# Optimization experiments

Hardware: AMD Instinct MI355X
Metric: run time of the kernel (lower is better)

The kernel has to match this reference:

```python
import jax, jax.numpy as jnp
import numpy as np

B, S, D, H, NS = 4, 4096, 1024, 16, 128
DA, DF = 512, 4096
DK, DV = DA // H, D // H  # 32, 64
TEMP = 1.0
EPS = 1e-6


def setup_inputs() -> dict:
    key = jax.random.key(0)
    ks = jax.random.split(key, 8)
    r = lambda k, shp: jax.random.normal(k, shp, jnp.float32) * 0.02
    return dict(
        x=jax.random.normal(ks[0], (B, S, D), jnp.float32),
        mask=jnp.ones((B, S), jnp.float32),
        residual_scale=jnp.ones((1,), jnp.float32),
        w_q=r(ks[1], (D, DA)), b_q=jnp.zeros((DA,), jnp.float32),
        w_kv=r(ks[2], (D, DA + D)), b_kv=jnp.zeros((DA + D,), jnp.float32),
        w_s=r(ks[3], (D, H * NS)), b_s=jnp.zeros((H * NS,), jnp.float32),
        w_cat=r(ks[4], (D, D)), b_cat=jnp.zeros((D,), jnp.float32),
        norm1_w=jnp.ones((D,), jnp.float32), norm2_w=jnp.ones((D,), jnp.float32),
        w1=r(ks[5], (D, DF)), b1=jnp.zeros((DF,), jnp.float32),
        w2=r(ks[6], (DF, D)), b2=jnp.zeros((D,), jnp.float32),
    )


def _rms(x, w):
    return x * jax.lax.rsqrt(jnp.mean(x * x, axis=-1, keepdims=True) + EPS) * w


def _forward(x, mask, residual_scale, w_q, b_q, w_kv, b_kv, w_s, b_s,
             w_cat, b_cat, norm1_w, norm2_w, w1, b1, w2, b2):
    neg = jnp.finfo(jnp.float32).min
    xn = _rms(x, norm1_w)
    q = (xn @ w_q + b_q).reshape(B, S, H, DK).transpose(0, 2, 1, 3)        # [B,H,S,DK]
    kv = (xn @ w_kv + b_kv).reshape(B, S, H, DK + DV).transpose(0, 2, 1, 3)  # [B,H,S,DK+DV]
    k_raw, v_raw = kv[..., :DK], kv[..., DK:]

    # DSZRC sampler: per-head soft routing of S tokens -> NS sampled KV rows
    logits = (x @ w_s + b_s).reshape(B, S, H, NS).transpose(0, 2, 3, 1)    # [B,H,NS,S]
    logits = jnp.where(mask[:, None, None, :] > 0, logits, neg)
    probs = jax.nn.softmax(logits / TEMP, axis=-1)
    kv_s = jnp.einsum('bhms,bhsd->bhmd', probs, kv)                        # [B,H,NS,DK+DV]
    k_s, v_s = kv_s[..., :DK], kv_s[..., DK:]

    # branch 1: dense SDPA over sampled KV
    scale = 1.0 / np.sqrt(DK).astype(np.float32)
    att = jax.nn.softmax(jnp.einsum('bhqd,bhkd->bhqk', q, k_s) * scale, axis=-1)
    out1 = jnp.einsum('bhqk,bhkd->bhqd', att, v_s)                         # [B,H,S,DV]

    # branch 2: fp16 sliding-window flash attn, left window = NS (keys i-NS..i)
    f16 = lambda t: t.astype(jnp.float16).astype(jnp.float32)
    qh, kh, vh = f16(q), f16(k_raw), f16(v_raw)
    bs = NS
    nb = S // bs
    qb = qh.reshape(B, H, nb, bs, DK)
    kb = kh.reshape(B, H, nb, bs, DK)
    vb = vh.reshape(B, H, nb, bs, DV)
    shift = lambda t: jnp.concatenate([jnp.zeros_like(t[:, :, :1]), t[:, :, :-1]], axis=2)
    kctx = jnp.concatenate([shift(kb), kb], axis=3)                        # [B,H,nb,2bs,DK]
    vctx = jnp.concatenate([shift(vb), vb], axis=3)
    sc = jnp.einsum('bhnad,bhnkd->bhnak', qb, kctx) * scale                # [B,H,nb,bs,2bs]
    a = jnp.arange(bs)[:, None]
    bcol = jnp.arange(2 * bs)[None, :]
    band = (bcol >= a) & (bcol <= a + NS)                                  # 0 <= q-k <= NS
    tpos = jnp.arange(nb)[:, None, None]
    valid = band[None] & ((tpos > 0) | (bcol >= bs)[None])                 # no keys before pos 0
    p = jax.nn.softmax(jnp.where(valid[None, None], sc, neg), axis=-1)
    out2 = f16(jnp.einsum('bhnak,bhnkd->bhnad', p, vctx)).reshape(B, H, S, DV)

    x_att = (out1 + out2).transpose(0, 2, 1, 3).reshape(B, S, D)
    x = x + (x_att @ w_cat + b_cat) * residual_scale
    h = _rms(x, norm2_w)
    x = x + (jax.nn.gelu(h @ w1 + b1, approximate=False) @ w2 + b2) * residual_scale
    return x


def reference(x, mask, residual_scale, w_q, b_q, w_kv, b_kv, w_s, b_s,
              w_cat, b_cat, norm1_w, norm2_w, w1, b1, w2, b2):
    return _forward(x, mask, residual_scale, w_q, b_q, w_kv, b_kv, w_s, b_s,
                    w_cat, b_cat, norm1_w, norm2_w, w1, b1, w2, b2)
```

## Files before the change

kernel.cpp:

```cpp
#include <hip/hip_runtime.h>
#include <cstdint>
#include <cmath>

#define DEV __device__ __forceinline__

using f16 = _Float16;
typedef f16  f16x4 __attribute__((ext_vector_type(4)));
typedef f16  f16x8 __attribute__((ext_vector_type(8)));
typedef float f32x4 __attribute__((ext_vector_type(4)));

constexpr int Bq = 4, Sq = 4096, Hq = 16;
constexpr int Tq = Bq * Sq;

DEV void gload_lds16(const void* g, void* l) {
  __builtin_amdgcn_global_load_lds(
      (const __attribute__((address_space(1))) void*)g,
      (__attribute__((address_space(3))) void*)l, 16, 0, 0);
}

DEV void stage_swz(const char* gbase, long gstride, char* lds, int nbytes,
                   int rowlog, int swzmask) {
  int tid = threadIdx.x;
  for (int b0 = 0; b0 < nbytes; b0 += 4096) {
    int P = b0 + tid * 16;
    int L = P ^ (((P >> rowlog) & swzmask) << 4);
    long row  = L >> rowlog;
    int  colb = L & ((1 << rowlog) - 1);
    gload_lds16(gbase + row * gstride + colb, lds + b0 + (tid & ~63) * 16);
  }
}

DEV void stage_swz512(const char* gbase, long gstride, char* lds, int nbytes,
                      int rowlog, int swzmask) {
  int tid = threadIdx.x;
  for (int b0 = 0; b0 < nbytes; b0 += 8192) {
    int P = b0 + tid * 16;
    int L = P ^ (((P >> rowlog) & swzmask) << 4);
    long row  = L >> rowlog;
    int  colb = L & ((1 << rowlog) - 1);
    gload_lds16(gbase + row * gstride + colb, lds + b0 + (tid & ~63) * 16);
  }
}

DEV float wave16_max(float v) {
#pragma unroll
  for (int d = 1; d < 16; d <<= 1) v = fmaxf(v, __shfl_xor(v, d, 64));
  return v;
}
DEV float wave16_sum(float v) {
#pragma unroll
  for (int d = 1; d < 16; d <<= 1) v += __shfl_xor(v, d, 64);
  return v;
}

__global__ __launch_bounds__(256) void wcast_k(const float* __restrict__ W,
                                               f16* __restrict__ Wt, int K, int N) {
  int n0 = blockIdx.x * 32, k0 = blockIdx.y * 32;
  __shared__ float tile[32][33];
  int tid = threadIdx.x, r = tid >> 5, c = tid & 31;
#pragma unroll
  for (int i = 0; i < 4; ++i)
    tile[r + i * 8][c] = W[(size_t)(k0 + r + i * 8) * N + n0 + c];
  __syncthreads();
#pragma unroll
  for (int i = 0; i < 4; ++i) {
    int rr = r + i * 8;
    Wt[(size_t)(n0 + rr) * K + k0 + c] = (f16)tile[c][rr];
  }
}

__global__ void bias_concat_k(const float* __restrict__ bq, const float* __restrict__ bkv,
                              float* __restrict__ out) {
  int i = blockIdx.x * 256 + threadIdx.x;
  out[i] = (i < 512) ? bq[i] : bkv[i - 512];
}

__global__ __launch_bounds__(256) void rmsnorm_k(const float* __restrict__ x,
                                                 const float* __restrict__ w,
                                                 f16* __restrict__ xn) {
  int row = blockIdx.x, tid = threadIdx.x;
  float4 v = ((const float4*)(x + (size_t)row * 1024))[tid];
  float ss = v.x * v.x + v.y * v.y + v.z * v.z + v.w * v.w;
#pragma unroll
  for (int d = 1; d < 64; d <<= 1) ss += __shfl_xor(ss, d, 64);
  __shared__ float red[4];
  if ((tid & 63) == 0) red[tid >> 6] = ss;
  __syncthreads();
  float tot = red[0] + red[1] + red[2] + red[3];
  float r = rsqrtf(tot * (1.0f / 1024.0f) + 1e-6f);
  float4 wv = ((const float4*)w)[tid];
  f16x4 o;
  o[0] = (f16)(v.x * r * wv.x); o[1] = (f16)(v.y * r * wv.y);
  o[2] = (f16)(v.z * r * wv.z); o[3] = (f16)(v.w * r * wv.w);
  *(f16x4*)(xn + (size_t)row * 1024 + tid * 4) = o;
}

template <int MODE>
__global__ __launch_bounds__(256) void gemm_k(const f16* __restrict__ A, const f16* __restrict__ Bt,
                                              const float* __restrict__ bias,
                                              float* __restrict__ outF,
                                              const float* __restrict__ resid,
                                              const float* __restrict__ rsp,
                                              int M, int N, int K, int lda, int ldb) {
  __shared__ alignas(16) char smA[2][16384];
  __shared__ alignas(16) char smB[2][16384];
  int nwgx = gridDim.x, nbc = gridDim.y;
  int bidl = blockIdx.y * nwgx + blockIdx.x;
  int cpx = (nwgx * nbc) >> 3;
  int xcd = bidl & 7, pos = bidl >> 3;
  int rpm = cpx / nbc;
  int nbi = pos / rpm, mbi = pos % rpm;
  int mb = xcd * rpm + mbi;
  long n0 = (long)nbi * 128;
  int tid = threadIdx.x, lane = tid & 63, wv = tid >> 6, wr = wv >> 1, wc = wv & 1;
  long m0 = (long)mb * 128;
  f32x4 acc[4][4] = {};

  const char* gA[4]; const char* gB[4]; int lo[4];
  long stepA = (MODE == 7) ? 524288 : 128;
  {
    const char* Abase;
    if (MODE == 7) Abase = (const char*)(A + (((m0 >> 12) * 16) * 4096 + (m0 & 4095)) * 64);
    else           Abase = (const char*)(A + m0 * lda);
    const char* Bbase = (const char*)(Bt + n0 * ldb);
    long astr = (MODE == 7) ? 128 : (long)lda * 2;
#pragma unroll
    for (int c = 0; c < 4; ++c) {
      int P = c * 4096 + tid * 16;
      int L = P ^ (((P >> 7) & 7) << 4);
      long row = L >> 7; int colb = L & 127;
      lo[c] = c * 4096 + (tid & ~63) * 16;
      gA[c] = Abase + row * astr + colb;
      gB[c] = Bbase + row * ((long)ldb * 2) + colb;
    }
  }
  auto stageAB = [&](int buf, int t) {
#pragma unroll
    for (int c = 0; c < 4; ++c) gload_lds16(gB[c] + (long)t * 128, smB[buf] + lo[c]);
#pragma unroll
    for (int c = 0; c < 4; ++c) gload_lds16(gA[c] + (long)t * stepA, smA[buf] + lo[c]);
  };

  int T = K >> 6;
  stageAB(0, 0);
  __syncthreads();
  int cur = 0;
  for (int t = 0; t < T; ++t) {
    if (t + 1 < T) stageAB(cur ^ 1, t + 1);
#pragma unroll
    for (int kk = 0; kk < 2; ++kk) {
      int kbyte = kk * 64 + (lane >> 4) * 16;
      f16x8 aF[4], bF[4];
#pragma unroll
      for (int m = 0; m < 4; ++m) {
        int L = (wr * 64 + m * 16 + (lane & 15)) * 128 + kbyte;
        aF[m] = *(const f16x8*)(smA[cur] + (L ^ (((L >> 7) & 7) << 4)));
      }
#pragma unroll
      for (int n = 0; n < 4; ++n) {
        int L = (wc * 64 + n * 16 + (lane & 15)) * 128 + kbyte;
        bF[n] = *(const f16x8*)(smB[cur] + (L ^ (((L >> 7) & 7) << 4)));
      }
#pragma unroll
      for (int m = 0; m < 4; ++m)
#pragma unroll
        for (int n = 0; n < 4; ++n)
          acc[m][n] = __builtin_amdgcn_mfma_f32_16x16x32_f16(aF[m], bF[n], acc[m][n], 0, 0, 0);
    }
    __syncthreads();
    cur ^= 1;
  }
  float rsv = rsp[0];
#pragma unroll
  for (int m = 0; m < 4; ++m)
#pragma unroll
    for (int n = 0; n < 4; ++n) {
      long gn = n0 + wc * 64 + n * 16 + (lane & 15);
      float bv = bias[gn];
      long rbase = m0 + wr * 64 + m * 16 + (lane >> 4) * 4;
#pragma unroll
      for (int i = 0; i < 4; ++i) {
        long gm = rbase + i;
        float v = acc[m][n][i] + bv;
        long idx = gm * N + gn;
        outF[idx] = resid[idx] + v * rsv;
      }
    }
}

template <int MODE>
__global__ __launch_bounds__(512) void gemm256_k(const f16* __restrict__ A, const f16* __restrict__ Bt,
                                                 const float* __restrict__ bias,
                                                 f16* __restrict__ o1, f16* __restrict__ o2,
                                                 f16* __restrict__ o3,
                                                 const float* __restrict__ resid,
                                                 int M, int N, int K, int lda, int ldb, int pp) {
  __shared__ alignas(16) char smA[2][32768];
  __shared__ alignas(16) char smB[2][32768];
  int nwgx = gridDim.x, nbc = gridDim.y;
  int bidl = blockIdx.y * nwgx + blockIdx.x;
  int cpx = (nwgx * nbc) >> 3;
  int xcd = bidl & 7, pos = bidl >> 3;
  int rpm = cpx / nbc;
  int nbi = pos / rpm, mbi = pos % rpm;
  int mb = xcd * rpm + mbi;
  long n0 = (long)nbi * 256;
  int tid = threadIdx.x, lane = tid & 63, wv = tid >> 6;
  int wr = wv >> 2, wc = wv & 3;
  long m0;
  long t0 = 0;
  int bq = 0;
  if (MODE == 5) {
    bq = mb >> 3; int sb = mb & 7;
    m0 = (long)sb * 256;
    t0 = (long)bq * 4096 + (long)pp * 2048 + m0;
  } else {
    m0 = (long)mb * 256;
  }
  f32x4 acc[8][4] = {};
  const char* Bb = (const char*)(Bt + n0 * ldb);

  if constexpr (MODE == 5) {
    auto stageAB5 = [&](int buf, int k0) {
      stage_swz512(Bb + (long)k0 * 2, (long)ldb * 2, smB[buf], 32768, 7, 7);
      int P = tid * 16;
#pragma unroll
      for (int b0 = 0; b0 < 32768; b0 += 8192) {
        int PP = b0 + P;
        int L = PP ^ (((PP >> 7) & 7) << 4);
        int row = L >> 7, colf = (L & 127) >> 1;
        const float* src = resid + (size_t)(t0 + row) * 1024 + k0 + colf;
        float4 u0 = *(const float4*)src;
        float4 u1 = *(const float4*)(src + 4);
        f16x8 o;
        o[0] = (f16)u0.x; o[1] = (f16)u0.y; o[2] = (f16)u0.z; o[3] = (f16)u0.w;
        o[4] = (f16)u1.x; o[5] = (f16)u1.y; o[6] = (f16)u1.z; o[7] = (f16)u1.w;
        *(f16x8*)(smA[buf] + PP) = o;
      }
    };
    stageAB5(0, 0);
    __syncthreads();
    int cur = 0;
    for (int k0 = 0; k0 < K; k0 += 64) {
      if (k0 + 64 < K) stageAB5(cur ^ 1, k0 + 64);
#pragma unroll
      for (int kk = 0; kk < 2; ++kk) {
        int kb2 = kk * 64 + (lane >> 4) * 16;
        f16x8 aF[8], bF[4];
#pragma unroll
        for (int m = 0; m < 8; ++m) {
          int L = (wr * 128 + m * 16 + (lane & 15)) * 128 + kb2;
          aF[m] = *(const f16x8*)(smA[cur] + (L ^ (((L >> 7) & 7) << 4)));
        }
#pragma unroll
        for (int n = 0; n < 4; ++n) {
          int L = (wc * 64 + n * 16 + (lane & 15)) * 128 + kb2;
          bF[n] = *(const f16x8*)(smB[cur] + (L ^ (((L >> 7) & 7) << 4)));
        }
#pragma unroll
        for (int m = 0; m < 8; ++m)
#pragma unroll
          for (int n = 0; n < 4; ++n)
            acc[m][n] = __builtin_amdgcn_mfma_f32_16x16x32_f16(aF[m], bF[n], acc[m][n], 0, 0, 0);
      }
      __syncthreads();
      cur ^= 1;
    }
  } else {
    const char* gA[4]; const char* gB[4]; int lo[4];
    {
      const char* Abase = (const char*)(A + m0 * lda);
#pragma unroll
      for (int c = 0; c < 4; ++c) {
        int P = c * 8192 + tid * 16;
        int L = P ^ (((P >> 7) & 7) << 4);
        long row = L >> 7; int colb = L & 127;
        lo[c] = c * 8192 + (tid & ~63) * 16;
        gA[c] = Abase + row * ((long)lda * 2) + colb;
        gB[c] = Bb + row * ((long)ldb * 2) + colb;
      }
    }
    auto stageAB = [&](int buf, int t) {
#pragma unroll
      for (int c = 0; c < 4; ++c) gload_lds16(gB[c] + (long)t * 128, smB[buf] + lo[c]);
#pragma unroll
      for (int c = 0; c < 4; ++c) gload_lds16(gA[c] + (long)t * 128, smA[buf] + lo[c]);
    };
    int T = K >> 6;
    stageAB(0, 0);
    __syncthreads();
    int cur = 0;
    for (int t = 0; t < T; ++t) {
      if (t + 1 < T) stageAB(cur ^ 1, t + 1);
#pragma unroll
      for (int kk = 0; kk < 2; ++kk) {
        int kb2 = kk * 64 + (lane >> 4) * 16;
        f16x8 aF[8], bF[4];
#pragma unroll
        for (int m = 0; m < 8; ++m) {
          int L = (wr * 128 + m * 16 + (lane & 15)) * 128 + kb2;
          aF[m] = *(const f16x8*)(smA[cur] + (L ^ (((L >> 7) & 7) << 4)));
        }
#pragma unroll
        for (int n = 0; n < 4; ++n) {
          int L = (wc * 64 + n * 16 + (lane & 15)) * 128 + kb2;
          bF[n] = *(const f16x8*)(smB[cur] + (L ^ (((L >> 7) & 7) << 4)));
        }
#pragma unroll
        for (int m = 0; m < 8; ++m)
#pragma unroll
          for (int n = 0; n < 4; ++n)
            acc[m][n] = __builtin_amdgcn_mfma_f32_16x16x32_f16(aF[m], bF[n], acc[m][n], 0, 0, 0);
      }
      __syncthreads();
      cur ^= 1;
    }
  }
#pragma unroll
  for (int m = 0; m < 8; ++m)
#pragma unroll
    for (int n = 0; n < 4; ++n) {
      long gn = n0 + wc * 64 + n * 16 + (lane & 15);
      float bv = bias[gn];
      long rbase = m0 + wr * 128 + m * 16 + (lane >> 4) * 4;
      if (MODE == 4) {
        long b = rbase >> 12, s = rbase & 4095;
        if (gn < 512) {
          long h = gn >> 5, dk = gn & 31;
#pragma unroll
          for (int i = 0; i < 4; ++i)
            o1[(((size_t)b * 16 + h) * 4096 + s + i) * 32 + dk] = (f16)(acc[m][n][i] + bv);
        } else {
          long c2 = gn - 512, h = c2 / 96, j = c2 % 96;
          if (j < 32) {
#pragma unroll
            for (int i = 0; i < 4; ++i)
              o2[(((size_t)b * 16 + h) * 4096 + s + i) * 32 + j] = (f16)(acc[m][n][i] + bv);
          } else {
            f16x4 pk;
#pragma unroll
            for (int i = 0; i < 4; ++i) pk[i] = (f16)(acc[m][n][i] + bv);
            *(f16x4*)(o3 + (((size_t)b * 16 + h) * 64 + (j - 32)) * 4096 + s) = pk;
          }
        }
      } else {
#pragma unroll
        for (int i = 0; i < 4; ++i) {
          long gm = rbase + i;
          float v = acc[m][n][i] + bv;
          if (MODE == 3) {
            float u = v * 0.7978845608028654f * (1.f + 0.044715f * v * v);
            float e = __expf(fminf(2.f * u, 80.f));
            o1[gm * N + gn] = (f16)(v * (e / (e + 1.f)));
          } else {
            o1[((size_t)bq * 2048 + gn) * 2048 + gm] = (f16)v;
          }
        }
      }
    }
}

__global__ __launch_bounds__(256) void kvs_k(const f16* __restrict__ lt,
                                             const f16* __restrict__ kh,
                                             const f16* __restrict__ vT,
                                             const float* __restrict__ mask,
                                             float* __restrict__ pacc, int pass) {
  int gx = blockIdx.x, nsb = gx & 3, sc = gx >> 2;
  int h = blockIdx.y, b = blockIdx.z;
  int bh = b * 16 + h;
  __shared__ alignas(16) char smA[4096];
  __shared__ alignas(16) f16 smB[112][88];
  int tid = threadIdx.x, lane = tid & 63, w = tid >> 6;
  int mf = w >> 1, nb0 = (w & 1) * 4, nfr = (w & 1) ? 3 : 4;
  for (int idx = tid; idx < 16 * 64; idx += 256) {
    int r = 96 + (idx >> 6), c2 = idx & 63;
    smB[r][c2] = (r == 96) ? (f16)1.0f : (f16)0.0f;
  }
  f32x4 acc[4] = {};
  const f16* ltb = lt + ((size_t)bh * 128 + nsb * 32) * 2048;
  for (int it = 0; it < 4; ++it) {
    int sl0 = sc * 256 + it * 64;
    int s0g = pass * 2048 + sl0;
    __syncthreads();
    {
      int P = tid * 16;
      int L = P ^ (((P >> 7) & 7) << 4);
      int row = L >> 7, colf = (L & 127) >> 1;
      f16x8 lv = *(const f16x8*)(ltb + (size_t)row * 2048 + sl0 + colf);
      const float* mrow = mask + (size_t)b * 4096 + s0g + colf;
      float4 m0v = *(const float4*)mrow, m1v = *(const float4*)(mrow + 4);
      float mm[8] = {m0v.x, m0v.y, m0v.z, m0v.w, m1v.x, m1v.y, m1v.z, m1v.w};
      f16x8 o;
#pragma unroll
      for (int j = 0; j < 8; ++j)
        o[j] = (f16)((mm[j] > 0.f) ? expf((float)lv[j] - 8.0f) : 0.0f);
      *(f16x8*)(smA + P) = o;
    }
    {
      int sl = tid >> 2, jg = (tid & 3) * 8;
      f16x8 u = *(const f16x8*)(kh + ((size_t)bh * 4096 + s0g + sl) * 32 + jg);
#pragma unroll
      for (int j = 0; j < 8; ++j) smB[jg + j][sl] = u[j];
    }
#pragma unroll
    for (int half = 0; half < 2; ++half) {
      int task = tid + half * 256;
      int dv = task >> 3, sl0v = (task & 7) * 8;
      f16x8 u = *(const f16x8*)(vT + ((size_t)bh * 64 + dv) * 4096 + s0g + sl0v);
      *(f16x8*)(&smB[32 + dv][sl0v]) = u;
    }
    __syncthreads();
#pragma unroll
    for (int kk = 0; kk < 2; ++kk) {
      int kbyte = kk * 64 + (lane >> 4) * 16;
      int L = (mf * 16 + (lane & 15)) * 128 + kbyte;
      f16x8 aF = *(const f16x8*)(smA + (L ^ (((L >> 7) & 7) << 4)));
#pragma unroll
      for (int n = 0; n < 4; ++n)
        if (n < nfr) {
          f16x8 bF = *(const f16x8*)((const char*)smB + ((nb0 + n) * 16 + (lane & 15)) * 176 + kbyte);
          acc[n] = __builtin_amdgcn_mfma_f32_16x16x32_f16(aF, bF, acc[n], 0, 0, 0);
        }
    }
  }
  int slot = pass * 8 + sc;
  float* pb = pacc + (((size_t)bh * 4 + nsb) * 16 + slot) * 3584;
#pragma unroll
  for (int n = 0; n < 4; ++n)
    if (n < nfr) {
      int col = (nb0 + n) * 16 + (lane & 15);
#pragma unroll
      for (int i = 0; i < 4; ++i) {
        int nsrow = mf * 16 + (lane >> 4) * 4 + i;
        pb[(size_t)nsrow * 112 + col] = acc[n][i];
      }
    }
}

__global__ __launch_bounds__(256) void kvs_fin_k(const float* __restrict__ pacc,
                                                 f16* __restrict__ ks, f16* __restrict__ vst) {
  int bh = blockIdx.x, tid = threadIdx.x;
  __shared__ float den[128];
  const float* base = pacc + (size_t)bh * 4 * 16 * 3584;
  if (tid < 128) {
    int nsb = tid >> 5, nsl = tid & 31;
    float d = 0.f;
#pragma unroll
    for (int slot = 0; slot < 16; ++slot)
      d += base[((size_t)nsb * 16 + slot) * 3584 + (size_t)nsl * 112 + 96];
    den[tid] = d;
  }
  __syncthreads();
  for (int e = tid; e < 12288; e += 256) {
    int ns = e / 96, j = e % 96;
    int nsb = ns >> 5, nsl = ns & 31;
    float sv = 0.f;
#pragma unroll
    for (int slot = 0; slot < 16; ++slot)
      sv += base[((size_t)nsb * 16 + slot) * 3584 + (size_t)nsl * 112 + j];
    float v = sv / den[ns];
    if (j < 32) ks[((size_t)bh * 128 + ns) * 32 + j] = (f16)v;
    else        vst[((size_t)bh * 64 + (j - 32)) * 128 + ns] = (f16)v;
  }
}

__global__ __launch_bounds__(256) void att_k(const f16* __restrict__ qh,
                                             const f16* __restrict__ kh,
                                             const f16* __restrict__ vTh,
                                             const f16* __restrict__ ksb,
                                             const f16* __restrict__ vstb,
                                             f16* __restrict__ xatt) {
  int ntj = blockIdx.x, h = blockIdx.y, b = blockIdx.z;
  int nt = ((ntj & 7) << 3) | (ntj >> 3);
  int bh = b * 16 + h, s0 = nt * 64;
  __shared__ alignas(16) char smQ[4096];
  __shared__ alignas(16) char smK[4096];
  __shared__ alignas(16) char smV[8192];
  __shared__ alignas(16) f16 smP[4][16][72];
  int tid = threadIdx.x, lane = tid & 63, w = tid >> 6;
  const float scale = 0.17677669529663687f;
  stage_swz((const char*)(qh + ((size_t)bh * 4096 + s0) * 32), 64, smQ, 4096, 6, 3);

  float mrun[4], lrun[4], m1[4], l1[4];
#pragma unroll
  for (int i = 0; i < 4; ++i) { mrun[i] = -1e30f; lrun[i] = 0.f; m1[i] = -1e30f; l1[i] = 0.f; }
  f32x4 o2[4] = {}, o1[4] = {};

  for (int c = 0; c < 5; ++c) {
    bool win = (c < 3);
    long kb = (long)s0 + (c - 2) * 64;
    if (win && kb < 0) continue;
    __syncthreads();
    if (win) {
      stage_swz((const char*)(kh + ((size_t)bh * 4096 + kb) * 32), 64, smK, 4096, 6, 3);
      stage_swz((const char*)(vTh + (size_t)bh * 64 * 4096 + kb), 8192, smV, 8192, 7, 7);
    } else {
      int sc = c - 3;
      stage_swz((const char*)(ksb + ((size_t)bh * 128 + sc * 64) * 32), 64, smK, 4096, 6, 3);
      stage_swz((const char*)(vstb + (size_t)bh * 64 * 128 + sc * 64), 256, smV, 8192, 7, 7);
    }
    __syncthreads();
    f32x4 s[4] = {};
    {
      int kbyte = (lane >> 4) * 16;
      int Lq = (w * 16 + (lane & 15)) * 64 + kbyte;
      f16x8 aF = *(const f16x8*)(smQ + (Lq ^ (((Lq >> 6) & 3) << 4)));
#pragma unroll
      for (int n = 0; n < 4; ++n) {
        int Lk = (n * 16 + (lane & 15)) * 64 + kbyte;
        f16x8 bF = *(const f16x8*)(smK + (Lk ^ (((Lk >> 6) & 3) << 4)));
        s[n] = __builtin_amdgcn_mfma_f32_16x16x32_f16(aF, bF, s[n], 0, 0, 0);
      }
    }
    float* mr = win ? mrun : m1;
    float* lr = win ? lrun : l1;
    f32x4* oo = win ? o2 : o1;
#pragma unroll
    for (int i = 0; i < 4; ++i) {
      int a2 = w * 16 + (lane >> 4) * 4 + i;
      float nm = mr[i];
#pragma unroll
      for (int n = 0; n < 4; ++n) {
        int kl = n * 16 + (lane & 15);
        bool valid = !win || (c == 1) || (c == 0 ? (kl >= a2) : (kl <= a2));
        float v = valid ? s[n][i] * scale : -1e30f;
        s[n][i] = v; nm = fmaxf(nm, v);
      }
      nm = wave16_max(nm);
      float alpha = expf(mr[i] - nm);
      float sum = 0.f;
#pragma unroll
      for (int n = 0; n < 4; ++n) { float p = expf(s[n][i] - nm); s[n][i] = p; sum += p; }
      sum = wave16_sum(sum);
      lr[i] = lr[i] * alpha + sum;
      mr[i] = nm;
#pragma unroll
      for (int n = 0; n < 4; ++n) oo[n][i] *= alpha;
    }
#pragma unroll
    for (int n = 0; n < 4; ++n)
#pragma unroll
      for (int i = 0; i < 4; ++i)
        smP[w][(lane >> 4) * 4 + i][n * 16 + (lane & 15)] = (f16)s[n][i];
#pragma unroll
    for (int kk = 0; kk < 2; ++kk) {
      int kb2 = kk * 64 + (lane >> 4) * 16;
      f16x8 aP = *(const f16x8*)((const char*)smP[w] + (lane & 15) * 144 + kb2);
#pragma unroll
      for (int n = 0; n < 4; ++n) {
        int dv = n * 16 + (lane & 15);
        int Lv = dv * 128 + kb2;
        f16x8 bV = *(const f16x8*)(smV + (Lv ^ (((Lv >> 7) & 7) << 4)));
        oo[n] = __builtin_amdgcn_mfma_f32_16x16x32_f16(aP, bV, oo[n], 0, 0, 0);
      }
    }
  }
  f16* xb = xatt + ((size_t)bh * 4096 + s0) * 64;
#pragma unroll
  for (int n = 0; n < 4; ++n)
#pragma unroll
    for (int i = 0; i < 4; ++i) {
      int row = w * 16 + (lane >> 4) * 4 + i, dv = n * 16 + (lane & 15);
      xb[(size_t)row * 64 + dv] = (f16)(o2[n][i] / lrun[i] + o1[n][i] / l1[i]);
    }
}

__global__ void sentinel_k(float* out, size_t n, float val) {
  size_t i = (size_t)blockIdx.x * 256 + threadIdx.x;
  size_t stride = (size_t)gridDim.x * 256;
  for (; i < n; i += stride) out[i] = val;
}

constexpr size_t OFF_WQKV = 0;
constexpr size_t OFF_WSC  = OFF_WQKV + 2048ull * 1024 * 2;
constexpr size_t OFF_WCAT = OFF_WSC  + 2048ull * 1024 * 2;
constexpr size_t OFF_W1   = OFF_WCAT + 1024ull * 1024 * 2;
constexpr size_t OFF_W2   = OFF_W1   + 4096ull * 1024 * 2;
constexpr size_t OFF_BQKV = OFF_W2   + 1024ull * 4096 * 2;
constexpr size_t OFF_ZB   = OFF_BQKV + 8192;
constexpr size_t OFF_Q    = OFF_ZB   + 4096;
constexpr size_t OFF_K    = OFF_Q    + (size_t)Tq * 512 * 2;
constexpr size_t OFF_P1   = OFF_K    + (size_t)Tq * 512 * 2;
constexpr size_t OFF_VT   = OFF_P1   + (size_t)Tq * 1024 * 2;
constexpr size_t OFF_KVA  = OFF_VT   + (size_t)Tq * 1024 * 2;
constexpr size_t OFF_KS   = OFF_KVA  + 64ull * 128 * 112 * 4;
constexpr size_t OFF_VST  = OFF_KS   + 64ull * 128 * 32 * 2;
constexpr size_t WS_NEED  = OFF_VST  + 64ull * 64 * 128 * 2;

extern "C" void kernel_launch(void* const* d_in, const int* in_sizes, int n_in,
                              void* d_out, int out_size, void* d_ws, size_t ws_size,
                              hipStream_t stream) {
  float* xo = (float*)d_out;
  if (ws_size < WS_NEED) {
    float val = -(1000.0f + (float)(ws_size / 1000000ull));
    sentinel_k<<<2048, 256, 0, stream>>>(xo, (size_t)out_size, val);
    return;
  }
  const float* x     = (const float*)d_in[0];
  const float* mask  = (const float*)d_in[1];
  const float* rsp   = (const float*)d_in[2];
  const float* w_q   = (const float*)d_in[3];
  const float* b_q   = (const float*)d_in[4];
  const float* w_kv  = (const float*)d_in[5];
  const float* b_kv  = (const float*)d_in[6];
  const float* w_s   = (const float*)d_in[7];
  const float* b_s   = (const float*)d_in[8];
  const float* w_cat = (const float*)d_in[9];
  const float* b_cat = (const float*)d_in[10];
  const float* n1w   = (const float*)d_in[11];
  const float* n2w   = (const float*)d_in[12];
  const float* w1    = (const float*)d_in[13];
  const float* b1    = (const float*)d_in[14];
  const float* w2    = (const float*)d_in[15];
  const float* b2    = (const float*)d_in[16];
  char* ws = (char*)d_ws;

  f16*   wqkv_t = (f16*)(ws + OFF_WQKV);
  f16*   ws_t   = (f16*)(ws + OFF_WSC);
  f16*   wcat_t = (f16*)(ws + OFF_WCAT);
  f16*   w1_t   = (f16*)(ws + OFF_W1);
  f16*   w2_t   = (f16*)(ws + OFF_W2);
  float* bqkv   = (float*)(ws + OFF_BQKV);
  f16*   q_h    = (f16*)(ws + OFF_Q);
  f16*   k_h    = (f16*)(ws + OFF_K);
  f16*   h_h    = (f16*)(ws + OFF_Q);
  f16*   xn_h   = (f16*)(ws + OFF_P1);
  f16*   lt16   = (f16*)(ws + OFF_P1);
  f16*   xatt_h = (f16*)(ws + OFF_P1);
  f16*   g_h    = (f16*)(ws + OFF_P1);
  f16*   vT_h   = (f16*)(ws + OFF_VT);
  f16*   ks_h   = (f16*)(ws + OFF_KS);
  f16*   vst_h  = (f16*)(ws + OFF_VST);

  wcast_k<<<dim3(16, 32),  256, 0, stream>>>(w_q,   wqkv_t,              1024, 512);
  wcast_k<<<dim3(48, 32),  256, 0, stream>>>(w_kv,  wqkv_t + 512 * 1024, 1024, 1536);
  wcast_k<<<dim3(64, 32),  256, 0, stream>>>(w_s,   ws_t,                1024, 2048);
  wcast_k<<<dim3(32, 32),  256, 0, stream>>>(w_cat, wcat_t,              1024, 1024);
  wcast_k<<<dim3(128, 32), 256, 0, stream>>>(w1,    w1_t,                1024, 4096);
  wcast_k<<<dim3(32, 128), 256, 0, stream>>>(w2,    w2_t,                4096, 1024);
  bias_concat_k<<<8, 256, 0, stream>>>(b_q, b_kv, bqkv);

  rmsnorm_k<<<Tq, 256, 0, stream>>>(x, n1w, xn_h);
  gemm256_k<4><<<dim3(64, 8), 512, 0, stream>>>(xn_h, wqkv_t, bqkv, q_h, k_h, vT_h,
                                                nullptr, Tq, 2048, 1024, 1024, 1024, 0);
  for (int p = 0; p < 2; ++p) {
    gemm256_k<5><<<dim3(32, 8), 512, 0, stream>>>(nullptr, ws_t, b_s, lt16, nullptr, nullptr,
                                                  x, 8192, 2048, 1024, 0, 1024, p);
    kvs_k<<<dim3(32, 16, 4), 256, 0, stream>>>(lt16, k_h, vT_h, mask, xo, p);
  }
  kvs_fin_k<<<64, 256, 0, stream>>>(xo, ks_h, vst_h);
  att_k<<<dim3(64, 16, 4), 256, 0, stream>>>(q_h, k_h, vT_h, ks_h, vst_h, xatt_h);
  gemm_k<7><<<dim3(128, 8), 256, 0, stream>>>(xatt_h, wcat_t, b_cat, xo,
                                              x, rsp, Tq, 1024, 1024, 0, 1024);
  rmsnorm_k<<<Tq, 256, 0, stream>>>(xo, n2w, h_h);
  for (int mc = 0; mc < 2; ++mc) {
    const f16* hA = h_h + (size_t)mc * 8192 * 1024;
    float* xoc = xo + (size_t)mc * 8192 * 1024;
    gemm256_k<3><<<dim3(32, 16), 512, 0, stream>>>(hA, w1_t, b1, g_h, nullptr, nullptr,
                                                   nullptr, 8192, 4096, 1024, 1024, 1024, 0);
    gemm_k<2><<<dim3(64, 8), 256, 0, stream>>>(g_h, w2_t, b2, xoc,
                                               xoc, rsp, 8192, 1024, 4096, 4096, 4096);
  }
}
```

Measured before the change: 928.6 us.

## Double-buffer K/V staging in attention and merge weight-cast launches

The attention kernel now keeps two LDS buffers for K and V and issues the async global-to-LDS load for the next chunk before computing the current one. This drops one barrier per chunk and lets memory traffic overlap with MFMA work. It also computes the starting chunk up front for the first tiles, where the old loop skipped them with continue. Separately, the six weight transpose-cast launches are merged into one kernel that dispatches on block index, cutting launch overhead. LDS use in att_k grows by 12KB, which may lower occupancy.

```diff
diff --git a/kernel.cpp b/kernel.cpp
--- a/kernel.cpp
+++ b/kernel.cpp
@@ -11,6 +11,22 @@
 
 constexpr int Bq = 4, Sq = 4096, Hq = 16;
 constexpr int Tq = Bq * Sq;
+
+constexpr size_t OFF_WQKV = 0;
+constexpr size_t OFF_WSC  = OFF_WQKV + 2048ull * 1024 * 2;
+constexpr size_t OFF_WCAT = OFF_WSC  + 2048ull * 1024 * 2;
+constexpr size_t OFF_W1   = OFF_WCAT + 1024ull * 1024 * 2;
+constexpr size_t OFF_W2   = OFF_W1   + 4096ull * 1024 * 2;
+constexpr size_t OFF_BQKV = OFF_W2   + 1024ull * 4096 * 2;
+constexpr size_t OFF_ZB   = OFF_BQKV + 8192;
+constexpr size_t OFF_Q    = OFF_ZB   + 4096;
+constexpr size_t OFF_K    = OFF_Q    + (size_t)Tq * 512 * 2;
+constexpr size_t OFF_P1   = OFF_K    + (size_t)Tq * 512 * 2;
+constexpr size_t OFF_VT   = OFF_P1   + (size_t)Tq * 1024 * 2;
+constexpr size_t OFF_KVA  = OFF_VT   + (size_t)Tq * 1024 * 2;
+constexpr size_t OFF_KS   = OFF_KVA  + 64ull * 128 * 112 * 4;
+constexpr size_t OFF_VST  = OFF_KS   + 64ull * 128 * 32 * 2;
+constexpr size_t WS_NEED  = OFF_VST  + 64ull * 64 * 128 * 2;
 
 DEV void gload_lds16(const void* g, void* l) {
   __builtin_amdgcn_global_load_lds(
@@ -53,9 +69,23 @@
   return v;
 }
 
-__global__ __launch_bounds__(256) void wcast_k(const float* __restrict__ W,
-                                               f16* __restrict__ Wt, int K, int N) {
-  int n0 = blockIdx.x * 32, k0 = blockIdx.y * 32;
+__global__ __launch_bounds__(256) void wcast_all_k(const float* __restrict__ w_q,
+                                                   const float* __restrict__ w_kv,
+                                                   const float* __restrict__ w_s,
+                                                   const float* __restrict__ w_cat,
+                                                   const float* __restrict__ w1,
+                                                   const float* __restrict__ w2,
+                                                   char* __restrict__ ws) {
+  int id = blockIdx.x;
+  const float* W; f16* Wt; int K, N, lid;
+  if (id < 512)        { W = w_q;   Wt = (f16*)(ws + OFF_WQKV);              K = 1024; N = 512;  lid = id; }
+  else if (id < 2048)  { W = w_kv;  Wt = (f16*)(ws + OFF_WQKV) + 512 * 1024; K = 1024; N = 1536; lid = id - 512; }
+  else if (id < 4096)  { W = w_s;   Wt = (f16*)(ws + OFF_WSC);               K = 1024; N = 2048; lid = id - 2048; }
+  else if (id < 5120)  { W = w_cat; Wt = (f16*)(ws + OFF_WCAT);              K = 1024; N = 1024; lid = id - 4096; }
+  else if (id < 9216)  { W = w1;    Wt = (f16*)(ws + OFF_W1);                K = 1024; N = 4096; lid = id - 5120; }
+  else                 { W = w2;    Wt = (f16*)(ws + OFF_W2);                K = 4096; N = 1024; lid = id - 9216; }
+  int ntx = N >> 5;
+  int n0 = (lid % ntx) * 32, k0 = (lid / ntx) * 32;
   __shared__ float tile[32][33];
   int tid = threadIdx.x, r = tid >> 5, c = tid & 31;
 #pragma unroll
@@ -474,32 +504,37 @@
   int nt = ((ntj & 7) << 3) | (ntj >> 3);
   int bh = b * 16 + h, s0 = nt * 64;
   __shared__ alignas(16) char smQ[4096];
-  __shared__ alignas(16) char smK[4096];
-  __shared__ alignas(16) char smV[8192];
+  __shared__ alignas(16) char smK[2][4096];
+  __shared__ alignas(16) char smV[2][8192];
   __shared__ alignas(16) f16 smP[4][16][72];
   int tid = threadIdx.x, lane = tid & 63, w = tid >> 6;
   const float scale = 0.17677669529663687f;
   stage_swz((const char*)(qh + ((size_t)bh * 4096 + s0) * 32), 64, smQ, 4096, 6, 3);
 
+  auto stage_chunk = [&](int c, int buf) {
+    if (c < 3) {
+      long kb = (long)s0 + (c - 2) * 64;
+      stage_swz((const char*)(kh + ((size_t)bh * 4096 + kb) * 32), 64, smK[buf], 4096, 6, 3);
+      stage_swz((const char*)(vTh + (size_t)bh * 64 * 4096 + kb), 8192, smV[buf], 8192, 7, 7);
+    } else {
+      int sc = c - 3;
+      stage_swz((const char*)(ksb + ((size_t)bh * 128 + sc * 64) * 32), 64, smK[buf], 4096, 6, 3);
+      stage_swz((const char*)(vstb + (size_t)bh * 64 * 128 + sc * 64), 256, smV[buf], 8192, 7, 7);
+    }
+  };
+
   float mrun[4], lrun[4], m1[4], l1[4];
 #pragma unroll
   for (int i = 0; i < 4; ++i) { mrun[i] = -1e30f; lrun[i] = 0.f; m1[i] = -1e30f; l1[i] = 0.f; }
   f32x4 o2[4] = {}, o1[4] = {};
 
-  for (int c = 0; c < 5; ++c) {
+  int c0 = (nt == 0) ? 2 : ((nt == 1) ? 1 : 0);
+  stage_chunk(c0, 0);
+  __syncthreads();
+  int cur = 0;
+  for (int c = c0; c < 5; ++c) {
+    if (c + 1 < 5) stage_chunk(c + 1, cur ^ 1);
     bool win = (c < 3);
-    long kb = (long)s0 + (c - 2) * 64;
-    if (win && kb < 0) continue;
-    __syncthreads();
-    if (win) {
-      stage_swz((const char*)(kh + ((size_t)bh * 4096 + kb) * 32), 64, smK, 4096, 6, 3);
-      stage_swz((const char*)(vTh + (size_t)bh * 64 * 4096 + kb), 8192, smV, 8192, 7, 7);
-    } else {
-      int sc = c - 3;
-      stage_swz((const char*)(ksb + ((size_t)bh * 128 + sc * 64) * 32), 64, smK, 4096, 6, 3);
-      stage_swz((const char*)(vstb + (size_t)bh * 64 * 128 + sc * 64), 256, smV, 8192, 7, 7);
-    }
-    __syncthreads();
     f32x4 s[4] = {};
     {
       int kbyte = (lane >> 4) * 16;
@@ -508,7 +543,7 @@
 #pragma unroll
       for (int n = 0; n < 4; ++n) {
         int Lk = (n * 16 + (lane & 15)) * 64 + kbyte;
-        f16x8 bF = *(const f16x8*)(smK + (Lk ^ (((Lk >> 6) & 3) << 4)));
+        f16x8 bF = *(const f16x8*)(smK[cur] + (Lk ^ (((Lk >> 6) & 3) << 4)));
         s[n] = __builtin_amdgcn_mfma_f32_16x16x32_f16(aF, bF, s[n], 0, 0, 0);
       }
     }
@@ -550,10 +585,12 @@
       for (int n = 0; n < 4; ++n) {
         int dv = n * 16 + (lane & 15);
         int Lv = dv * 128 + kb2;
-        f16x8 bV = *(const f16x8*)(smV + (Lv ^ (((Lv >> 7) & 7) << 4)));
+        f16x8 bV = *(const f16x8*)(smV[cur] + (Lv ^ (((Lv >> 7) & 7) << 4)));
         oo[n] = __builtin_amdgcn_mfma_f32_16x16x32_f16(aP, bV, oo[n], 0, 0, 0);
       }
     }
+    __syncthreads();
+    cur ^= 1;
   }
   f16* xb = xatt + ((size_t)bh * 4096 + s0) * 64;
 #pragma unroll
@@ -570,22 +607,6 @@
   size_t stride = (size_t)gridDim.x * 256;
   for (; i < n; i += stride) out[i] = val;
 }
-
-constexpr size_t OFF_WQKV = 0;
-constexpr size_t OFF_WSC  = OFF_WQKV + 2048ull * 1024 * 2;
-constexpr size_t OFF_WCAT = OFF_WSC  + 2048ull * 1024 * 2;
-constexpr size_t OFF_W1   = OFF_WCAT + 1024ull * 1024 * 2;
-constexpr size_t OFF_W2   = OFF_W1   + 4096ull * 1024 * 2;
-constexpr size_t OFF_BQKV = OFF_W2   + 1024ull * 4096 * 2;
-constexpr size_t OFF_ZB   = OFF_BQKV + 8192;
-constexpr size_t OFF_Q    = OFF_ZB   + 4096;
-constexpr size_t OFF_K    = OFF_Q    + (size_t)Tq * 512 * 2;
-constexpr size_t OFF_P1   = OFF_K    + (size_t)Tq * 512 * 2;
-constexpr size_t OFF_VT   = OFF_P1   + (size_t)Tq * 1024 * 2;
-constexpr size_t OFF_KVA  = OFF_VT   + (size_t)Tq * 1024 * 2;
-constexpr size_t OFF_KS   = OFF_KVA  + 64ull * 128 * 112 * 4;
-constexpr size_t OFF_VST  = OFF_KS   + 64ull * 128 * 32 * 2;
-constexpr size_t WS_NEED  = OFF_VST  + 64ull * 64 * 128 * 2;
 
 extern "C" void kernel_launch(void* const* d_in, const int* in_sizes, int n_in,
                               void* d_out, int out_size, void* d_ws, size_t ws_size,
@@ -632,12 +653,7 @@
   f16*   ks_h   = (f16*)(ws + OFF_KS);
   f16*   vst_h  = (f16*)(ws + OFF_VST);
 
-  wcast_k<<<dim3(16, 32),  256, 0, stream>>>(w_q,   wqkv_t,              1024, 512);
-  wcast_k<<<dim3(48, 32),  256, 0, stream>>>(w_kv,  wqkv_t + 512 * 1024, 1024, 1536);
-  wcast_k<<<dim3(64, 32),  256, 0, stream>>>(w_s,   ws_t,                1024, 2048);
-  wcast_k<<<dim3(32, 32),  256, 0, stream>>>(w_cat, wcat_t,              1024, 1024);
-  wcast_k<<<dim3(128, 32), 256, 0, stream>>>(w1,    w1_t,                1024, 4096);
-  wcast_k<<<dim3(32, 128), 256, 0, stream>>>(w2,    w2_t,                4096, 1024);
+  wcast_all_k<<<13312, 256, 0, stream>>>(w_q, w_kv, w_s, w_cat, w1, w2, ws);
   bias_concat_k<<<8, 256, 0, stream>>>(b_q, b_kv, bqkv);
 
   rmsnorm_k<<<Tq, 256, 0, stream>>>(x, n1w, xn_h);
```

Result: no change. 941.4 us (+1.4%).
